# Kernel tuning notes

Measured on AMD Instinct MI355X. Metric: run time of the kernel, lower is better.

Reference implementation:

```python
import jax, jax.numpy as jnp
import numpy as np

BETA = 0.25
DECAY = 0.99
EPS = 1e-05


def setup_inputs() -> dict:
    key = jax.random.key(0)
    k1, k2, k3, k4 = jax.random.split(key, 4)
    B, D, T, N = 8, 256, 1024, 16384
    return {
        "z": jax.random.normal(k1, (B, D, T), dtype=jnp.float32),
        "weight": jax.random.normal(k2, (N, D), dtype=jnp.float32),
        "cluster_size": jax.random.uniform(k3, (N,), dtype=jnp.float32),
        "embed_avg": jax.random.normal(k4, (N, D), dtype=jnp.float32),
    }


def reference(z, weight, cluster_size, embed_avg):
    # z: [B, D, T] -> [B, T, D]
    B, D, T = z.shape
    N = weight.shape[0]
    zp = jnp.transpose(z, (0, 2, 1))            # [B, T, D]
    zf = zp.reshape(-1, D)                      # [BT, D]

    # squared-distance matrix: ||z||^2 + ||w||^2 - 2 z.w  -> [BT, N]
    d = (jnp.sum(zf * zf, axis=1, keepdims=True)
         + jnp.sum(weight * weight, axis=1)
         - 2.0 * jnp.einsum('bd,nd->bn', zf, weight))
    idx = jnp.argmin(d, axis=1)                 # [BT]

    z_q = weight[idx].reshape(B, T, D)          # codebook gather

    # perplexity from code-usage histogram (== mean of one-hot encodings)
    counts = jnp.zeros((N,), dtype=zf.dtype).at[idx].add(1.0)
    avg_probs = counts / idx.shape[0]
    perplexity = jnp.exp(-jnp.sum(avg_probs * jnp.log(avg_probs + 1e-10)))

    # EMA codebook update (training path; scatter-add of assigned vectors)
    embed_sum = jnp.zeros_like(weight).at[idx].add(zf)   # encodings^T @ zf
    new_cluster_size = DECAY * cluster_size + (1.0 - DECAY) * counts
    new_embed_avg = DECAY * embed_avg + (1.0 - DECAY) * embed_sum
    n = jnp.sum(new_cluster_size)
    smoothed = (new_cluster_size + EPS) / (n + N * EPS) * n
    new_weight = new_embed_avg / smoothed[:, None]

    # commitment loss + straight-through estimator
    loss = BETA * jnp.mean((jax.lax.stop_gradient(z_q) - zp) ** 2)
    z_q_st = zp + jax.lax.stop_gradient(z_q - zp)
    out = jnp.transpose(z_q_st, (0, 2, 1))      # back to [B, D, T]

    return (out, perplexity, idx, loss, new_weight, new_cluster_size, new_embed_avg)
```

## Files before the change

kernel.cpp:

```cpp
#include <hip/hip_runtime.h>
#include <hip/hip_bf16.h>


#define B_ 8
#define D_ 256
#define T_ 1024
#define BT_ 8192
#define N_ 16384

#define O_OUT   0
#define O_PERP  2097152
#define O_IDX   2097153
#define O_LOSS  2105345
#define O_NEWW  2105346
#define O_NCS   6299650
#define O_NEA   6316034

#define W_CNT   0ull
#define W_SCAL  65536ull
#define W_W2    98560ull
#define W_IDXI  164096ull
#define W_PACK  196864ull
#define W_ZH    1245440ull
#define W_WH    5439744ull
#define W_ZT    13828352ull

typedef __attribute__((ext_vector_type(8))) _Float16 half8;
typedef __attribute__((ext_vector_type(4))) _Float16 half4;
typedef __attribute__((ext_vector_type(4))) float f32x4;

__device__ __forceinline__ void gl_lds(const void* g, void* l) {
  __builtin_amdgcn_global_load_lds(
      (const __attribute__((address_space(1))) unsigned int*)g,
      (__attribute__((address_space(3))) unsigned int*)l, 16, 0, 0);
}

__device__ __forceinline__ unsigned sortable(float f) {
  unsigned u = __float_as_uint(f);
  return u ^ (((unsigned)((int)u >> 31)) | 0x80000000u);
}

__global__ void k_prepz_r13(const float* __restrict__ z, _Float16* __restrict__ zh,
                            float* __restrict__ zt) {
  __shared__ float tile[64][65];
  const int t0 = blockIdx.x << 6, d0 = blockIdx.y << 6, b = blockIdx.z;
  const int tt = threadIdx.x & 63, q = threadIdx.x >> 6;
  for (int i = 0; i < 16; ++i) {
    const int dd = q + (i << 2);
    tile[tt][dd] = z[((size_t)b * D_ + d0 + dd) * T_ + t0 + tt];
  }
  __syncthreads();
  for (int i = 0; i < 16; ++i) {
    const int ttw = q + (i << 2);
    const float v = tile[ttw][tt];
    const size_t off = ((size_t)(b * T_ + t0 + ttw)) * D_ + d0 + tt;
    zh[off] = (_Float16)v;
    zt[off] = v;
  }
}

__global__ void k_prepw_r8(const float* __restrict__ w, _Float16* __restrict__ wh,
                           float* __restrict__ w2) {
  const int row = blockIdx.x * 4 + (threadIdx.x >> 6);
  const int lane = threadIdx.x & 63;
  const float4 v = reinterpret_cast<const float4*>(w + (size_t)row * D_)[lane];
  half4 h;
  h[0] = (_Float16)v.x; h[1] = (_Float16)v.y; h[2] = (_Float16)v.z; h[3] = (_Float16)v.w;
  *reinterpret_cast<half4*>(wh + (size_t)row * D_ + (lane << 2)) = h;
  float s = v.x * v.x + v.y * v.y + v.z * v.z + v.w * v.w;
  for (int o = 32; o; o >>= 1) s += __shfl_xor(s, o);
  if (lane == 0) w2[row] = s;
}

__global__ __launch_bounds__(512, 4) void k_dist_r12(
    const _Float16* __restrict__ zh, const _Float16* __restrict__ wh,
    const float* __restrict__ w2, unsigned long long* __restrict__ pack) {
  __shared__ _Float16 As[2][8192];
  __shared__ _Float16 Bs[2][8192];
  __shared__ unsigned long long Ms[2][128][2];

  const int tid = threadIdx.x;
  const int lane = tid & 63, w = tid >> 6;
  const int quad = lane >> 4, l15 = lane & 15;
  const int r0 = blockIdx.x << 7;
  const int cy = blockIdx.y;
  const int nbase = cy << 11;
  const int wrow = (w & 3) << 5;
  const int wcol = (w >> 2) << 6;

  int smj[2], scj[2];
#pragma unroll
  for (int j = 0; j < 2; ++j) {
    const int slot = ((w << 1) + j) * 64 + lane;
    smj[j] = slot >> 3;
    scj[j] = (slot & 7) ^ (smj[j] & 7);
  }

  float rd0[8], rd1[8];
  int ri0[8], ri1[8];
#pragma unroll
  for (int s = 0; s < 8; ++s) { rd0[s] = 3.0e38f; rd1[s] = 3.0e38f; ri0[s] = 0; ri1[s] = 0; }

#pragma unroll
  for (int j = 0; j < 2; ++j) {
    gl_lds(zh + (((size_t)(r0 + smj[j])) << 8) + (scj[j] << 3),
           &As[0][(((w << 1) + j) * 64 + lane) << 3]);
    gl_lds(wh + (((size_t)(nbase + smj[j])) << 8) + (scj[j] << 3),
           &Bs[0][(((w << 1) + j) * 64 + lane) << 3]);
  }

  f32x4 acc[2][4];
  float w2h[4];

#pragma unroll 1
  for (int ct = 0; ct < 16; ++ct) {
    const int n0 = nbase + (ct << 7);
#pragma unroll
    for (int kc = 0; kc < 4; ++kc) {
      const int cur = kc & 1;
      __syncthreads();
      if (kc < 3) {
#pragma unroll
        for (int j = 0; j < 2; ++j) {
          gl_lds(zh + (((size_t)(r0 + smj[j])) << 8) + ((kc + 1) << 6) + (scj[j] << 3),
                 &As[cur ^ 1][(((w << 1) + j) * 64 + lane) << 3]);
          gl_lds(wh + (((size_t)(n0 + smj[j])) << 8) + ((kc + 1) << 6) + (scj[j] << 3),
                 &Bs[cur ^ 1][(((w << 1) + j) * 64 + lane) << 3]);
        }
      } else if (ct < 15) {
        const int n0n = n0 + 128;
#pragma unroll
        for (int j = 0; j < 2; ++j) {
          gl_lds(zh + (((size_t)(r0 + smj[j])) << 8) + (scj[j] << 3),
                 &As[cur ^ 1][(((w << 1) + j) * 64 + lane) << 3]);
          gl_lds(wh + (((size_t)(n0n + smj[j])) << 8) + (scj[j] << 3),
                 &Bs[cur ^ 1][(((w << 1) + j) * 64 + lane) << 3]);
        }
      }
      if (kc == 0) {
#pragma unroll
        for (int cf = 0; cf < 4; ++cf) w2h[cf] = 0.5f * w2[n0 + wcol + cf * 16 + l15];
#pragma unroll
        for (int i = 0; i < 2; ++i)
#pragma unroll
          for (int j = 0; j < 4; ++j) acc[i][j] = (f32x4)(0.f);
      }
#pragma unroll
      for (int kl = 0; kl < 2; ++kl) {
        const int k8 = (kl << 2) + quad;
        half8 af[2], bf[4];
#pragma unroll
        for (int rf = 0; rf < 2; ++rf) {
          const int m = wrow + rf * 16 + l15;
          af[rf] = *reinterpret_cast<const half8*>(&As[cur][(m << 6) + ((k8 ^ (m & 7)) << 3)]);
        }
#pragma unroll
        for (int cf = 0; cf < 4; ++cf) {
          const int n = wcol + cf * 16 + l15;
          bf[cf] = *reinterpret_cast<const half8*>(&Bs[cur][(n << 6) + ((k8 ^ (n & 7)) << 3)]);
        }
#pragma unroll
        for (int rf = 0; rf < 2; ++rf)
#pragma unroll
          for (int cf = 0; cf < 4; ++cf)
            acc[rf][cf] = __builtin_amdgcn_mfma_f32_16x16x32_f16(af[rf], bf[cf], acc[rf][cf], 0, 0, 0);
      }
      if (kc == 3) {
#pragma unroll
        for (int rf = 0; rf < 2; ++rf)
#pragma unroll
          for (int cf = 0; cf < 4; ++cf) {
            const int idxv = n0 + wcol + cf * 16 + l15;
#pragma unroll
            for (int rg = 0; rg < 4; ++rg) {
              const int s = rf * 4 + rg;
              const float d = w2h[cf] - acc[rf][cf][rg];
              if (d < rd1[s]) {
                if (d < rd0[s]) { rd1[s] = rd0[s]; ri1[s] = ri0[s]; rd0[s] = d; ri0[s] = idxv; }
                else { rd1[s] = d; ri1[s] = idxv; }
              }
            }
          }
      }
    }
  }

#pragma unroll
  for (int s = 0; s < 8; ++s) {
    unsigned long long p0 = ((unsigned long long)sortable(rd0[s]) << 32) | (unsigned int)ri0[s];
    unsigned long long p1 = ((unsigned long long)sortable(rd1[s]) << 32) | (unsigned int)ri1[s];
    for (int off = 1; off < 16; off <<= 1) {
      const unsigned long long q0 = __shfl_xor(p0, off);
      const unsigned long long q1 = __shfl_xor(p1, off);
      const unsigned long long lo = p0 < q0 ? p0 : q0;
      const unsigned long long mx = p0 < q0 ? q0 : p0;
      const unsigned long long mn1 = p1 < q1 ? p1 : q1;
      p0 = lo;
      p1 = mx < mn1 ? mx : mn1;
    }
    if (l15 == 0) {
      const int row = wrow + (s >> 2) * 16 + quad * 4 + (s & 3);
      Ms[w >> 2][row][0] = p0;
      Ms[w >> 2][row][1] = p1;
    }
  }
  __syncthreads();
  if (tid < 128) {
    const unsigned long long a0 = Ms[0][tid][0], a1 = Ms[0][tid][1];
    const unsigned long long b0 = Ms[1][tid][0], b1 = Ms[1][tid][1];
    const unsigned long long p0 = a0 < b0 ? a0 : b0;
    const unsigned long long p1 = a0 < b0 ? (a1 < b0 ? a1 : b0) : (b1 < a0 ? b1 : a0);
    unsigned long long* dst = pack + (((size_t)(r0 + tid)) << 4) + (cy << 1);
    dst[0] = p0;
    dst[1] = p1;
  }
}

__global__ void k_cand_r13(const float* __restrict__ zt, const float* __restrict__ weight,
                           const unsigned long long* __restrict__ pack,
                           int* __restrict__ idxi, float* __restrict__ counts,
                           float* __restrict__ oidx, float* __restrict__ loss_acc) {
  __shared__ float lred[4];
  const int wv_ = threadIdx.x >> 6;
  const int row = blockIdx.x * 4 + wv_;
  const int lane = threadIdx.x & 63;
  const int g = lane >> 4, l = lane & 15;

  float4 zc[4];
#pragma unroll
  for (int q = 0; q < 4; ++q)
    zc[q] = reinterpret_cast<const float4*>(zt + (size_t)row * D_)[(q << 4) + l];

  double best = 1.0e300;
  int bestid = 0x7FFFFFFF;
#pragma unroll
  for (int c = 0; c < 4; ++c) {
    const int cand = (int)(pack[((size_t)row << 4) + (g << 2) + c] & 0xFFFFFFFFull) & 16383;
    double s = 0.0;
#pragma unroll
    for (int q = 0; q < 4; ++q) {
      const float4 wvv = reinterpret_cast<const float4*>(weight + (size_t)cand * D_)[(q << 4) + l];
      const double d0 = (double)zc[q].x - (double)wvv.x;
      const double d1 = (double)zc[q].y - (double)wvv.y;
      const double d2 = (double)zc[q].z - (double)wvv.z;
      const double d3 = (double)zc[q].w - (double)wvv.w;
      s = fma(d0, d0, s); s = fma(d1, d1, s); s = fma(d2, d2, s); s = fma(d3, d3, s);
    }
    for (int o = 1; o < 16; o <<= 1) s += __shfl_xor(s, o);
    if (s < best || (s == best && cand < bestid)) { best = s; bestid = cand; }
  }
#pragma unroll
  for (int o = 16; o < 64; o <<= 1) {
    const double os = __shfl_xor(best, o);
    const int oi = __shfl_xor(bestid, o);
    if (os < best || (os == best && oi < bestid)) { best = os; bestid = oi; }
  }
  if (lane == 0) {
    idxi[row] = bestid;
    oidx[row] = (float)bestid;
    atomicAdd(&counts[bestid], 1.0f);
    lred[wv_] = (float)best;
  }
  __syncthreads();
  if (threadIdx.x == 0)
    atomicAdd(loss_acc, lred[0] + lred[1] + lred[2] + lred[3]);
}

__global__ void k_gather_r8(const float* __restrict__ weight, const int* __restrict__ idxi,
                            float* __restrict__ oout) {
  __shared__ float tile[32][257];
  __shared__ int ids[32];
  const int b = blockIdx.y, t0 = blockIdx.x << 5;
  const int lane = threadIdx.x & 63, wave = threadIdx.x >> 6;
  if (threadIdx.x < 32) ids[threadIdx.x] = idxi[b * T_ + t0 + threadIdx.x] & 16383;
  __syncthreads();
  for (int i = 0; i < 8; ++i) {
    const int tl = (wave << 3) + i;
    const float4 v = reinterpret_cast<const float4*>(weight + (size_t)ids[tl] * D_)[lane];
    tile[tl][(lane << 2) + 0] = v.x;
    tile[tl][(lane << 2) + 1] = v.y;
    tile[tl][(lane << 2) + 2] = v.z;
    tile[tl][(lane << 2) + 3] = v.w;
  }
  __syncthreads();
  const int tp = threadIdx.x & 31, dg = threadIdx.x >> 5;
  for (int it = 0; it < 32; ++it) {
    const int d = (dg << 5) + it;
    oout[((size_t)b * D_ + d) * T_ + t0 + tp] = tile[tp][d];
  }
}

__global__ void k_neainit_r9(const float* __restrict__ ea, float* __restrict__ onea) {
  const int i = blockIdx.x * 256 + threadIdx.x;
  const float4 v = reinterpret_cast<const float4*>(ea)[i];
  float4 o;
  o.x = 0.99f * v.x; o.y = 0.99f * v.y; o.z = 0.99f * v.z; o.w = 0.99f * v.w;
  reinterpret_cast<float4*>(onea)[i] = o;
}

__global__ void k_scatter_r8(const float* __restrict__ z, const int* __restrict__ idxi,
                             float* __restrict__ onea) {
  __shared__ float lds[64][65];
  __shared__ int ids[64];
  const int blk = blockIdx.x;
  const int b = blk >> 4, t0 = (blk & 15) << 6;
  const int lane = threadIdx.x & 63, w = threadIdx.x >> 6;
  if (threadIdx.x < 64) ids[threadIdx.x] = idxi[b * T_ + t0 + threadIdx.x] & 16383;
  for (int dc = 0; dc < D_; dc += 64) {
    __syncthreads();
    for (int i = 0; i < 16; ++i) {
      const int dd = (w << 4) + i;
      lds[dd][lane] = z[((size_t)b * D_ + dc + dd) * T_ + t0 + lane];
    }
    __syncthreads();
    for (int i = 0; i < 16; ++i) {
      const int tl = (w << 4) + i;
      atomicAdd(&onea[(size_t)ids[tl] * D_ + dc + lane], 0.01f * lds[lane][tl]);
    }
  }
}

__global__ void k_fincnt_r8(const float* __restrict__ cs, const float* __restrict__ counts,
                            float* __restrict__ oncs, float* __restrict__ ent_acc,
                            float* __restrict__ ntot_acc) {
  __shared__ float red[8];
  const int n = blockIdx.x * 256 + threadIdx.x;
  const float c = counts[n];
  const float ncs = 0.99f * cs[n] + 0.01f * c;
  oncs[n] = ncs;
  const float p = c * (1.0f / 8192.0f);
  float se = p * logf(p + 1e-10f);
  float sn = ncs;
  for (int o = 32; o; o >>= 1) {
    se += __shfl_xor(se, o);
    sn += __shfl_xor(sn, o);
  }
  const int lane = threadIdx.x & 63, wave = threadIdx.x >> 6;
  if (lane == 0) { red[wave] = se; red[4 + wave] = sn; }
  __syncthreads();
  if (threadIdx.x == 0) {
    atomicAdd(ent_acc, red[0] + red[1] + red[2] + red[3]);
    atomicAdd(ntot_acc, red[4] + red[5] + red[6] + red[7]);
  }
}

__global__ void k_finw_r8(const float* __restrict__ cs, const float* __restrict__ counts,
                          const float* __restrict__ ntot_acc,
                          const float* __restrict__ onea, float* __restrict__ oneww) {
  const int n = blockIdx.x;
  const int dl = threadIdx.x << 1;
  const float2 a = *reinterpret_cast<const float2*>(onea + (size_t)n * D_ + dl);
  const float ncs = 0.99f * cs[n] + 0.01f * counts[n];
  const float ntot = *ntot_acc;
  const float sm = (ncs + 1e-5f) / (ntot + N_ * 1e-5f) * ntot;
  float2 ow;
  ow.x = a.x / sm;
  ow.y = a.y / sm;
  *reinterpret_cast<float2*>(oneww + (size_t)n * D_ + dl) = ow;
}

__global__ void k_scal_r8(const float* __restrict__ loss_acc, const float* __restrict__ ent_acc,
                          float* __restrict__ operp, float* __restrict__ oloss) {
  if (threadIdx.x == 0) {
    *operp = expf(-*ent_acc);
    *oloss = 0.25f * (*loss_acc) * (1.0f / 2097152.0f);
  }
}

extern "C" void kernel_launch(void* const* d_in, const int* in_sizes, int n_in,
                              void* d_out, int out_size, void* d_ws, size_t ws_size,
                              hipStream_t stream) {
  (void)in_sizes; (void)n_in; (void)out_size; (void)ws_size;
  const float* z = (const float*)d_in[0];
  const float* weight = (const float*)d_in[1];
  const float* cs = (const float*)d_in[2];
  const float* ea = (const float*)d_in[3];
  float* out = (float*)d_out;
  char* ws = (char*)d_ws;

  float* counts = (float*)(ws + W_CNT);
  float* scal = (float*)(ws + W_SCAL);
  float* w2 = (float*)(ws + W_W2);
  int* idxi = (int*)(ws + W_IDXI);
  unsigned long long* pack = (unsigned long long*)(ws + W_PACK);
  _Float16* zh = (_Float16*)(ws + W_ZH);
  _Float16* wh = (_Float16*)(ws + W_WH);
  float* zt = (float*)(ws + W_ZT);

  hipMemsetAsync(ws + W_CNT, 0, 65792, stream);

  hipLaunchKernelGGL(k_prepz_r13, dim3(16, 4, 8), dim3(256), 0, stream, z, zh, zt);
  hipLaunchKernelGGL(k_prepw_r8, dim3(N_ / 4), dim3(256), 0, stream, weight, wh, w2);
  hipLaunchKernelGGL(k_dist_r12, dim3(64, 8), dim3(512), 0, stream, zh, wh, w2, pack);
  hipLaunchKernelGGL(k_cand_r13, dim3(BT_ / 4), dim3(256), 0, stream, zt, weight, pack,
                     idxi, counts, out + O_IDX, scal + 0);
  hipLaunchKernelGGL(k_gather_r8, dim3(32, 8), dim3(256), 0, stream, weight, idxi, out + O_OUT);
  hipLaunchKernelGGL(k_fincnt_r8, dim3(64), dim3(256), 0, stream, cs, counts, out + O_NCS,
                     scal + 1, scal + 2);
  hipLaunchKernelGGL(k_neainit_r9, dim3(N_ * D_ / 1024), dim3(256), 0, stream, ea, out + O_NEA);
  hipLaunchKernelGGL(k_scatter_r8, dim3(128), dim3(256), 0, stream, z, idxi, out + O_NEA);
  hipLaunchKernelGGL(k_finw_r8, dim3(N_), dim3(128), 0, stream, cs, counts, scal + 2,
                     out + O_NEA, out + O_NEWW);
  hipLaunchKernelGGL(k_scal_r8, dim3(1), dim3(64), 0, stream, scal + 0, scal + 1,
                     out + O_PERP, out + O_LOSS);
}
```

Measured before the change: 268.2 us.

## Widen distance tile to 1024 threads with resident A, fuse small kernels

The distance kernel now runs 1024 threads per block. It keeps the whole 128x256 fp16 z tile resident in LDS and loads it once, and it processes 256 codebook columns per iteration, so A is no longer reloaded for every column tile. The final top-2 merge now combines four wave groups instead of two. The separate EMA-init kernel is fused into the z transpose prep kernel, and the scalar finalisation is folded into the final weight kernel, which removes two launches. The larger LDS footprint and 1024-thread blocks lower occupancy and raise register pressure, which could hurt latency hiding.

Measured after the change: 263.0 us. Within noise of the previous version (-1.9%).

```diff
diff --git a/kernel.cpp b/kernel.cpp
--- a/kernel.cpp
+++ b/kernel.cpp
@@ -40,14 +40,26 @@
   return u ^ (((unsigned)((int)u >> 31)) | 0x80000000u);
 }
 
-__global__ void k_prepz_r13(const float* __restrict__ z, _Float16* __restrict__ zh,
-                            float* __restrict__ zt) {
+__global__ void k_prepz_r14(const float* __restrict__ z, _Float16* __restrict__ zh,
+                            float* __restrict__ zt, const float* __restrict__ ea,
+                            float* __restrict__ onea) {
   __shared__ float tile[64][65];
   const int t0 = blockIdx.x << 6, d0 = blockIdx.y << 6, b = blockIdx.z;
   const int tt = threadIdx.x & 63, q = threadIdx.x >> 6;
   for (int i = 0; i < 16; ++i) {
     const int dd = q + (i << 2);
     tile[tt][dd] = z[((size_t)b * D_ + d0 + dd) * T_ + t0 + tt];
+  }
+  const int bid = blockIdx.x + (blockIdx.y << 4) + (blockIdx.z << 6);
+  const float4* eav = reinterpret_cast<const float4*>(ea);
+  float4* ov = reinterpret_cast<float4*>(onea);
+#pragma unroll
+  for (int i = 0; i < 8; ++i) {
+    const int idx = (bid << 11) + (i << 8) + threadIdx.x;
+    const float4 v = eav[idx];
+    float4 o;
+    o.x = 0.99f * v.x; o.y = 0.99f * v.y; o.z = 0.99f * v.z; o.w = 0.99f * v.w;
+    ov[idx] = o;
   }
   __syncthreads();
   for (int i = 0; i < 16; ++i) {
@@ -72,12 +84,12 @@
   if (lane == 0) w2[row] = s;
 }
 
-__global__ __launch_bounds__(512, 4) void k_dist_r12(
+__global__ __launch_bounds__(1024, 4) void k_dist_r14(
     const _Float16* __restrict__ zh, const _Float16* __restrict__ wh,
     const float* __restrict__ w2, unsigned long long* __restrict__ pack) {
-  __shared__ _Float16 As[2][8192];
-  __shared__ _Float16 Bs[2][8192];
-  __shared__ unsigned long long Ms[2][128][2];
+  __shared__ _Float16 Asr[4][8192];
+  __shared__ _Float16 Bs[2][16384];
+  __shared__ unsigned long long Ms[4][128][2];
 
   const int tid = threadIdx.x;
   const int lane = tid & 63, w = tid >> 6;
@@ -88,54 +100,51 @@
   const int wrow = (w & 3) << 5;
   const int wcol = (w >> 2) << 6;
 
-  int smj[2], scj[2];
+  const int m_a = tid >> 3, cg_a = (tid & 7) ^ ((tid >> 3) & 7);
+#pragma unroll
+  for (int kc = 0; kc < 4; ++kc)
+    gl_lds(zh + (((size_t)(r0 + m_a)) << 8) + (kc << 6) + (cg_a << 3),
+           &Asr[kc][tid << 3]);
+
+  int smb[2], scb[2];
 #pragma unroll
   for (int j = 0; j < 2; ++j) {
-    const int slot = ((w << 1) + j) * 64 + lane;
-    smj[j] = slot >> 3;
-    scj[j] = (slot & 7) ^ (smj[j] & 7);
-  }
+    const int s = tid + (j << 10);
+    smb[j] = s >> 3;
+    scb[j] = (s & 7) ^ (smb[j] & 7);
+  }
+#pragma unroll
+  for (int j = 0; j < 2; ++j)
+    gl_lds(wh + (((size_t)(nbase + smb[j])) << 8) + (scb[j] << 3),
+           &Bs[0][(tid + (j << 10)) << 3]);
 
   float rd0[8], rd1[8];
   int ri0[8], ri1[8];
 #pragma unroll
   for (int s = 0; s < 8; ++s) { rd0[s] = 3.0e38f; rd1[s] = 3.0e38f; ri0[s] = 0; ri1[s] = 0; }
 
-#pragma unroll
-  for (int j = 0; j < 2; ++j) {
-    gl_lds(zh + (((size_t)(r0 + smj[j])) << 8) + (scj[j] << 3),
-           &As[0][(((w << 1) + j) * 64 + lane) << 3]);
-    gl_lds(wh + (((size_t)(nbase + smj[j])) << 8) + (scj[j] << 3),
-           &Bs[0][(((w << 1) + j) * 64 + lane) << 3]);
-  }
-
   f32x4 acc[2][4];
   float w2h[4];
 
 #pragma unroll 1
-  for (int ct = 0; ct < 16; ++ct) {
-    const int n0 = nbase + (ct << 7);
+  for (int ct = 0; ct < 8; ++ct) {
+    const int n0 = nbase + (ct << 8);
 #pragma unroll
     for (int kc = 0; kc < 4; ++kc) {
       const int cur = kc & 1;
       __syncthreads();
       if (kc < 3) {
-#pragma unroll
-        for (int j = 0; j < 2; ++j) {
-          gl_lds(zh + (((size_t)(r0 + smj[j])) << 8) + ((kc + 1) << 6) + (scj[j] << 3),
-                 &As[cur ^ 1][(((w << 1) + j) * 64 + lane) << 3]);
-          gl_lds(wh + (((size_t)(n0 + smj[j])) << 8) + ((kc + 1) << 6) + (scj[j] << 3),
-                 &Bs[cur ^ 1][(((w << 1) + j) * 64 + lane) << 3]);
-        }
-      } else if (ct < 15) {
-        const int n0n = n0 + 128;
-#pragma unroll
-        for (int j = 0; j < 2; ++j) {
-          gl_lds(zh + (((size_t)(r0 + smj[j])) << 8) + (scj[j] << 3),
-                 &As[cur ^ 1][(((w << 1) + j) * 64 + lane) << 3]);
-          gl_lds(wh + (((size_t)(n0n + smj[j])) << 8) + (scj[j] << 3),
-                 &Bs[cur ^ 1][(((w << 1) + j) * 64 + lane) << 3]);
-        }
+        const int kb = (kc + 1) << 6;
+#pragma unroll
+        for (int j = 0; j < 2; ++j)
+          gl_lds(wh + (((size_t)(n0 + smb[j])) << 8) + kb + (scb[j] << 3),
+                 &Bs[cur ^ 1][(tid + (j << 10)) << 3]);
+      } else if (ct < 7) {
+        const int n0n = n0 + 256;
+#pragma unroll
+        for (int j = 0; j < 2; ++j)
+          gl_lds(wh + (((size_t)(n0n + smb[j])) << 8) + (scb[j] << 3),
+                 &Bs[cur ^ 1][(tid + (j << 10)) << 3]);
       }
       if (kc == 0) {
 #pragma unroll
@@ -152,7 +161,7 @@
 #pragma unroll
         for (int rf = 0; rf < 2; ++rf) {
           const int m = wrow + rf * 16 + l15;
-          af[rf] = *reinterpret_cast<const half8*>(&As[cur][(m << 6) + ((k8 ^ (m & 7)) << 3)]);
+          af[rf] = *reinterpret_cast<const half8*>(&Asr[kc][(m << 6) + ((k8 ^ (m & 7)) << 3)]);
         }
 #pragma unroll
         for (int cf = 0; cf < 4; ++cf) {
@@ -206,10 +215,15 @@
   }
   __syncthreads();
   if (tid < 128) {
-    const unsigned long long a0 = Ms[0][tid][0], a1 = Ms[0][tid][1];
-    const unsigned long long b0 = Ms[1][tid][0], b1 = Ms[1][tid][1];
-    const unsigned long long p0 = a0 < b0 ? a0 : b0;
-    const unsigned long long p1 = a0 < b0 ? (a1 < b0 ? a1 : b0) : (b1 < a0 ? b1 : a0);
+    unsigned long long p0 = Ms[0][tid][0], p1 = Ms[0][tid][1];
+#pragma unroll
+    for (int g = 1; g < 4; ++g) {
+      const unsigned long long q0 = Ms[g][tid][0], q1 = Ms[g][tid][1];
+      const unsigned long long n0_ = p0 < q0 ? p0 : q0;
+      const unsigned long long n1_ = p0 < q0 ? (p1 < q0 ? p1 : q0) : (q1 < p0 ? q1 : p0);
+      p0 = n0_;
+      p1 = n1_;
+    }
     unsigned long long* dst = pack + (((size_t)(r0 + tid)) << 4) + (cy << 1);
     dst[0] = p0;
     dst[1] = p1;
@@ -288,14 +302,6 @@
     const int d = (dg << 5) + it;
     oout[((size_t)b * D_ + d) * T_ + t0 + tp] = tile[tp][d];
   }
-}
-
-__global__ void k_neainit_r9(const float* __restrict__ ea, float* __restrict__ onea) {
-  const int i = blockIdx.x * 256 + threadIdx.x;
-  const float4 v = reinterpret_cast<const float4*>(ea)[i];
-  float4 o;
-  o.x = 0.99f * v.x; o.y = 0.99f * v.y; o.z = 0.99f * v.z; o.w = 0.99f * v.w;
-  reinterpret_cast<float4*>(onea)[i] = o;
 }
 
 __global__ void k_scatter_r8(const float* __restrict__ z, const int* __restrict__ idxi,
@@ -344,9 +350,12 @@
   }
 }
 
-__global__ void k_finw_r8(const float* __restrict__ cs, const float* __restrict__ counts,
-                          const float* __restrict__ ntot_acc,
-                          const float* __restrict__ onea, float* __restrict__ oneww) {
+__global__ void k_finw_r14(const float* __restrict__ cs, const float* __restrict__ counts,
+                           const float* __restrict__ ntot_acc,
+                           const float* __restrict__ onea, float* __restrict__ oneww,
+                           const float* __restrict__ loss_acc,
+                           const float* __restrict__ ent_acc,
+                           float* __restrict__ operp, float* __restrict__ oloss) {
   const int n = blockIdx.x;
   const int dl = threadIdx.x << 1;
   const float2 a = *reinterpret_cast<const float2*>(onea + (size_t)n * D_ + dl);
@@ -357,11 +366,7 @@
   ow.x = a.x / sm;
   ow.y = a.y / sm;
   *reinterpret_cast<float2*>(oneww + (size_t)n * D_ + dl) = ow;
-}
-
-__global__ void k_scal_r8(const float* __restrict__ loss_acc, const float* __restrict__ ent_acc,
-                          float* __restrict__ operp, float* __restrict__ oloss) {
-  if (threadIdx.x == 0) {
+  if (n == 0 && threadIdx.x == 0) {
     *operp = expf(-*ent_acc);
     *oloss = 0.25f * (*loss_acc) * (1.0f / 2097152.0f);
   }
@@ -389,18 +394,17 @@
 
   hipMemsetAsync(ws + W_CNT, 0, 65792, stream);
 
-  hipLaunchKernelGGL(k_prepz_r13, dim3(16, 4, 8), dim3(256), 0, stream, z, zh, zt);
+  hipLaunchKernelGGL(k_prepz_r14, dim3(16, 4, 8), dim3(256), 0, stream, z, zh, zt,
+                     ea, out + O_NEA);
   hipLaunchKernelGGL(k_prepw_r8, dim3(N_ / 4), dim3(256), 0, stream, weight, wh, w2);
-  hipLaunchKernelGGL(k_dist_r12, dim3(64, 8), dim3(512), 0, stream, zh, wh, w2, pack);
+  hipLaunchKernelGGL(k_dist_r14, dim3(64, 8), dim3(1024), 0, stream, zh, wh, w2, pack);
   hipLaunchKernelGGL(k_cand_r13, dim3(BT_ / 4), dim3(256), 0, stream, zt, weight, pack,
                      idxi, counts, out + O_IDX, scal + 0);
   hipLaunchKernelGGL(k_gather_r8, dim3(32, 8), dim3(256), 0, stream, weight, idxi, out + O_OUT);
   hipLaunchKernelGGL(k_fincnt_r8, dim3(64), dim3(256), 0, stream, cs, counts, out + O_NCS,
                      scal + 1, scal + 2);
-  hipLaunchKernelGGL(k_neainit_r9, dim3(N_ * D_ / 1024), dim3(256), 0, stream, ea, out + O_NEA);
   hipLaunchKernelGGL(k_scatter_r8, dim3(128), dim3(256), 0, stream, z, idxi, out + O_NEA);
-  hipLaunchKernelGGL(k_finw_r8, dim3(N_), dim3(128), 0, stream, cs, counts, scal + 2,
-                     out + O_NEA, out + O_NEWW);
-  hipLaunchKernelGGL(k_scal_r8, dim3(1), dim3(64), 0, stream, scal + 0, scal + 1,
+  hipLaunchKernelGGL(k_finw_r14, dim3(N_), dim3(128), 0, stream, cs, counts, scal + 2,
+                     out + O_NEA, out + O_NEWW, scal + 0, scal + 1,
                      out + O_PERP, out + O_LOSS);
 }
```
